# Optimization experiments

Hardware: AMD Instinct MI355X
Metric: run time of the kernel (lower is better)

The kernel has to match this reference:

```python
import jax, jax.numpy as jnp
import numpy as np

SEQ_LEN, BATCH, NUM_GROUPS, GROUP = 12, 512, 16, 32
H, E, MLP, BOTTLE, PRE = 128, 64, 1024, 1024, 512


def _pool_net(h, pos, num_groups, Wp, bp, W1, b1, W2, b2):
    # PoolHiddenNet: for each scene group, pairwise relative positions -> MLP -> max over neighbors
    B = h.shape[0]
    G = B // num_groups
    hg = h.reshape(num_groups, G, -1)          # (NG, G, H)
    pg = pos.reshape(num_groups, G, 2)         # (NG, G, 2)
    rel = pg[:, None, :, :] - pg[:, :, None, :]  # [g,i,j] = pos_j - pos_i
    emb = rel @ Wp.T + bp                      # (NG, G, G, E)
    hj = jnp.broadcast_to(hg[:, None, :, :], (num_groups, G, G, hg.shape[-1]))
    feats = jnp.concatenate([emb, hj], axis=-1)  # (NG, G, G, E+H)
    x = jax.nn.relu(feats @ W1.T + b1)         # (NG, G, G, 512)
    x = jax.nn.relu(x @ W2.T + b2)             # (NG, G, G, 1024)
    return x.max(axis=2).reshape(B, -1)        # max over neighbors j


def setup_inputs() -> dict:
    key = jax.random.key(0)
    ks = jax.random.split(key, 24)
    s = 0.05
    starts = np.arange(NUM_GROUPS, dtype=np.int64) * GROUP
    seq_start_end = jnp.asarray(np.stack([starts, starts + GROUP], axis=1))
    return {
        "last_pos": jax.random.normal(ks[0], (BATCH, 2), jnp.float32),
        "last_pos_rel": jax.random.normal(ks[1], (BATCH, 2), jnp.float32),
        "hh": jax.random.normal(ks[2], (1, BATCH, H), jnp.float32),
        "ch": jax.random.normal(ks[3], (1, BATCH, H), jnp.float32),
        "pred_traj_rel": jax.random.normal(ks[4], (SEQ_LEN, BATCH, 2), jnp.float32),
        "seq_start_end": seq_start_end,
        # LSTM (torch layout: gates ordered i,f,g,o)
        "W_ih": jax.random.normal(ks[5], (4 * H, E), jnp.float32) * s,
        "W_hh": jax.random.normal(ks[6], (4 * H, H), jnp.float32) * s,
        "b_ih": jax.random.normal(ks[7], (4 * H,), jnp.float32) * s,
        "b_hh": jax.random.normal(ks[8], (4 * H,), jnp.float32) * s,
        # spatial_embedding Linear(2, E)
        "Wse": jax.random.normal(ks[9], (E, 2), jnp.float32) * s,
        "bse": jax.random.normal(ks[10], (E,), jnp.float32) * s,
        # hidden2pos Linear(H, 2)
        "Wpos": jax.random.normal(ks[11], (2, H), jnp.float32) * s,
        "bpos": jax.random.normal(ks[12], (2,), jnp.float32) * s,
        # pool_net spatial_embedding Linear(2, E)
        "Wp": jax.random.normal(ks[13], (E, 2), jnp.float32) * s,
        "bp": jax.random.normal(ks[14], (E,), jnp.float32) * s,
        # pool_net mlp_pre_pool: [E+H, 512, BOTTLE], relu after each linear
        "W1": jax.random.normal(ks[15], (PRE, E + H), jnp.float32) * s,
        "b1": jax.random.normal(ks[16], (PRE,), jnp.float32) * s,
        "W2": jax.random.normal(ks[17], (BOTTLE, PRE), jnp.float32) * s,
        "b2": jax.random.normal(ks[18], (BOTTLE,), jnp.float32) * s,
        # decoder mlp: [H+BOTTLE, MLP, H], relu after each linear
        "Wm1": jax.random.normal(ks[19], (MLP, H + BOTTLE), jnp.float32) * s,
        "bm1": jax.random.normal(ks[20], (MLP,), jnp.float32) * s,
        "Wm2": jax.random.normal(ks[21], (H, MLP), jnp.float32) * s,
        "bm2": jax.random.normal(ks[22], (H,), jnp.float32) * s,
    }


def reference(last_pos, last_pos_rel, hh, ch, pred_traj_rel, seq_start_end,
              W_ih, W_hh, b_ih, b_hh, Wse, bse, Wpos, bpos,
              Wp, bp, W1, b1, W2, b2, Wm1, bm1, Wm2, bm2):
    num_groups = seq_start_end.shape[0]
    h0, c0 = hh[0], ch[0]
    dec_in0 = last_pos_rel @ Wse.T + bse

    def step(carry, gt_rel):
        last_pos_c, h, c, dec_in, loss = carry
        # single-layer LSTM cell (torch gate order i,f,g,o)
        gates = dec_in @ W_ih.T + b_ih + h @ W_hh.T + b_hh
        i, f, g, o = jnp.split(gates, 4, axis=-1)
        c = jax.nn.sigmoid(f) * c + jax.nn.sigmoid(i) * jnp.tanh(g)
        h = jax.nn.sigmoid(o) * jnp.tanh(c)
        rel_pos = h @ Wpos.T + bpos
        curr_pos = rel_pos + last_pos_c
        # pool every timestep + mlp back down to h_dim, replaces hidden state
        pool_h = _pool_net(h, curr_pos, num_groups, Wp, bp, W1, b1, W2, b2)
        dh = jnp.concatenate([h, pool_h], axis=1)
        dh = jax.nn.relu(dh @ Wm1.T + bm1)
        h = jax.nn.relu(dh @ Wm2.T + bm2)
        # training mode: teacher forcing + MSE loss
        loss = loss + jnp.mean((rel_pos - gt_rel) ** 2)
        dec_in = gt_rel @ Wse.T + bse
        return (curr_pos, h, c, dec_in, loss), rel_pos

    init = (last_pos, h0, c0, dec_in0, jnp.float32(0.0))
    (_, _, _, _, loss), pred_traj = jax.lax.scan(step, init, pred_traj_rel)
    return pred_traj, loss
```

## Files before the change

kernel.cpp:

```cpp
#include <hip/hip_runtime.h>
#include <math.h>

#define BATCH 512
#define NG 16
#define GSZ 32
#define H 128
#define E 64
#define PRE 512
#define BOT 1024
#define MLPD 1024
#define SEQ 12
#define AK 1152

typedef __attribute__((ext_vector_type(8))) short bf16x8;
typedef __attribute__((ext_vector_type(4))) float f32x4;

union bf8pack { ushort s[8]; uint4 v; };

__device__ __forceinline__ unsigned short f2bf(float f) {
    unsigned u = __float_as_uint(f);
    u += 0x7FFF + ((u >> 16) & 1);
    return (unsigned short)(u >> 16);
}

#define GLB(p) ((const __attribute__((address_space(1))) unsigned int*)(p))
#define LDS(p) ((__attribute__((address_space(3))) unsigned int*)(p))

#define N0 (BOT * PRE)
#define N1 (MLPD * AK)
#define N2 (H * MLPD)
#define N3 (PRE * H)
#define N4 (PRE)
#define N5 (BATCH * H)
#define N5b (BATCH * H)
#define N6 (BATCH * 2)
#define N7 (512 * 128)
#define N8 (512)
#define PREP_TOT (N0 + N1 + N2 + N3 + N4 + N5 + N5b + N6 + N7 + N8 + 1)

__global__ void prep_kernel(
    const float* __restrict__ W2, const float* __restrict__ Wm1,
    const float* __restrict__ Wm2, const float* __restrict__ W1,
    const float* __restrict__ Wp, const float* __restrict__ bp, const float* __restrict__ b1,
    const float* __restrict__ ch, const float* __restrict__ hh, const float* __restrict__ last_pos,
    const float* __restrict__ Wih, const float* __restrict__ Whh,
    const float* __restrict__ bih, const float* __restrict__ bhh,
    const float* __restrict__ Wse, const float* __restrict__ bse,
    unsigned short* __restrict__ W2pk, unsigned short* __restrict__ Wm1pk,
    unsigned short* __restrict__ Wm2pk, unsigned short* __restrict__ W1pk,
    float* __restrict__ Wcx, float* __restrict__ Wcy, float* __restrict__ biash,
    float* __restrict__ cbuf, float* __restrict__ hbuf, float* __restrict__ pos,
    unsigned short* __restrict__ Whpk,
    float* __restrict__ Wx0, float* __restrict__ Wx1, float* __restrict__ bx,
    float* __restrict__ loss)
{
    long idx = (long)blockIdx.x * 256 + threadIdx.x;
    if (idx < N0) {
        int e = (int)(idx & 7);
        long u = idx >> 3;
        int lane = (int)(u & 63);
        int rest = (int)(u >> 6);
        int ksg = rest & 15, cg = rest >> 4;
        int col = cg * 16 + (lane & 15);
        int kk = ksg * 32 + (lane >> 4) * 8 + e;
        W2pk[idx] = f2bf(W2[(size_t)col * PRE + kk]);
        return;
    }
    idx -= N0;
    if (idx < N1) {
        int e = (int)(idx & 7);
        long u = idx >> 3;
        int lane = (int)(u & 63);
        long rest = u >> 6;
        int ksg = (int)(rest % 36);
        int cg = (int)(rest / 36);
        int col = cg * 16 + (lane & 15);
        int k = ksg * 32 + (lane >> 4) * 8 + e;
        Wm1pk[idx] = f2bf(Wm1[(size_t)col * AK + k]);
        return;
    }
    idx -= N1;
    if (idx < N2) {
        int e = (int)(idx & 7);
        long u = idx >> 3;
        int lane = (int)(u & 63);
        int rest = (int)(u >> 6);
        int ksg = rest & 31, cg = rest >> 5;
        int col = cg * 16 + (lane & 15);
        int k = ksg * 32 + (lane >> 4) * 8 + e;
        Wm2pk[idx] = f2bf(Wm2[(size_t)col * MLPD + k]);
        return;
    }
    idx -= N2;
    if (idx < N3) {
        int e = (int)(idx & 7);
        int u = (int)(idx >> 3);
        int l16 = u & 15, quad = (u >> 4) & 3, nt = (u >> 6) & 3, ks = (u >> 8) & 3, w = u >> 10;
        int col = w * 64 + nt * 16 + l16;
        int k = ks * 32 + quad * 8 + e;
        W1pk[idx] = f2bf(W1[col * 192 + E + k]);
        return;
    }
    idx -= N3;
    if (idx < N4) {
        int p = (int)idx;
        float sx = 0.f, sy = 0.f, sb = 0.f;
#pragma unroll 8
        for (int e = 0; e < E; ++e) {
            float w = W1[p * 192 + e];
            sx += w * Wp[e * 2 + 0];
            sy += w * Wp[e * 2 + 1];
            sb += w * bp[e];
        }
        Wcx[p] = sx; Wcy[p] = sy; biash[p] = b1[p] + sb;
        return;
    }
    idx -= N4;
    if (idx < N5) { cbuf[idx] = ch[idx]; return; }
    idx -= N5;
    if (idx < N5b) { hbuf[idx] = hh[idx]; return; }
    idx -= N5b;
    if (idx < N6) { pos[idx] = last_pos[idx]; return; }
    idx -= N6;
    if (idx < N7) {
        int e = (int)(idx & 7);
        int u = (int)(idx >> 3);
        int l16 = u & 15, quad = (u >> 4) & 3, ks = (u >> 6) & 3, w = (u >> 8) & 7, g = u >> 11;
        int col = g * 128 + w * 16 + l16;
        int k = ks * 32 + quad * 8 + e;
        Whpk[idx] = f2bf(Whh[col * H + k]);
        return;
    }
    idx -= N7;
    if (idx < N8) {
        int u = (int)idx;
        float sx = 0.f, sy = 0.f, sb = 0.f;
#pragma unroll 8
        for (int e = 0; e < E; ++e) {
            float w = Wih[u * E + e];
            sx += w * Wse[e * 2 + 0];
            sy += w * Wse[e * 2 + 1];
            sb += w * bse[e];
        }
        Wx0[u] = sx; Wx1[u] = sy; bx[u] = sb + bih[u] + bhh[u];
        return;
    }
    idx -= N8;
    if (idx == 0) *loss = 0.0f;
}

#define LROWS 16
__global__ __launch_bounds__(512) void lstm_hpart(
    int t,
    const float* __restrict__ relin, const float* __restrict__ gt,
    const unsigned short* __restrict__ Whpk,
    const float* __restrict__ Wx0, const float* __restrict__ Wx1, const float* __restrict__ bx,
    const float* __restrict__ Wpos, const float* __restrict__ bpos,
    const unsigned short* __restrict__ W1pk, const float* __restrict__ biash,
    const float* __restrict__ hbuf, float* __restrict__ cbuf,
    unsigned short* __restrict__ Abf, float* __restrict__ Hpartf,
    float* __restrict__ pos, float* __restrict__ traj, float* __restrict__ loss)
{
    constexpr int LDHB = 136;
    constexpr int LDHF = 129;
    __shared__ __align__(16) unsigned short As[LROWS * LDHB];
    __shared__ __align__(16) unsigned short hnb[LROWS * LDHB];
    __shared__ float hnf[LROWS * LDHF];
    __shared__ float lred[8];
    const int r0 = blockIdx.x * LROWS;
    const int tid = threadIdx.x;
    const int lane = tid & 63, w = tid >> 6;
    const int quad = lane >> 4, l16 = lane & 15;

    for (int idx = tid; idx < LROWS * H; idx += 512) {
        int row = idx >> 7, k = idx & 127;
        As[row * LDHB + k] = f2bf(hbuf[(size_t)(r0 + row) * H + k]);
    }
    __syncthreads();

    f32x4 acc[4];
#pragma unroll
    for (int g4 = 0; g4 < 4; ++g4) acc[g4] = (f32x4)0.f;
#pragma unroll
    for (int ks = 0; ks < 4; ++ks) {
        bf16x8 af = *(const bf16x8*)&As[l16 * LDHB + ks * 32 + quad * 8];
#pragma unroll
        for (int gate = 0; gate < 4; ++gate) {
            bf16x8 bf = *(const bf16x8*)&Whpk[((size_t)((gate * 8 + w) * 4 + ks) * 64 + lane) * 8];
            acc[gate] = __builtin_amdgcn_mfma_f32_16x16x32_bf16(af, bf, acc[gate], 0, 0, 0);
        }
    }

    {
        int u = w * 16 + l16;
        float wx0[4], wx1[4], bxv[4];
#pragma unroll
        for (int gate = 0; gate < 4; ++gate) {
            int col = gate * 128 + u;
            wx0[gate] = Wx0[col]; wx1[gate] = Wx1[col]; bxv[gate] = bx[col];
        }
#pragma unroll
        for (int r = 0; r < 4; ++r) {
            int row = quad * 4 + r;
            int b = r0 + row;
            float rx = relin[b * 2 + 0], ry = relin[b * 2 + 1];
            float i_ = acc[0][r] + rx * wx0[0] + ry * wx1[0] + bxv[0];
            float f_ = acc[1][r] + rx * wx0[1] + ry * wx1[1] + bxv[1];
            float g_ = acc[2][r] + rx * wx0[2] + ry * wx1[2] + bxv[2];
            float o_ = acc[3][r] + rx * wx0[3] + ry * wx1[3] + bxv[3];
            float ig = 1.0f / (1.0f + expf(-i_));
            float fg = 1.0f / (1.0f + expf(-f_));
            float gg = tanhf(g_);
            float og = 1.0f / (1.0f + expf(-o_));
            float c = fg * cbuf[(size_t)b * H + u] + ig * gg;
            cbuf[(size_t)b * H + u] = c;
            float h = og * tanhf(c);
            hnb[row * LDHB + u] = f2bf(h);
            hnf[row * LDHF + u] = h;
            Abf[(size_t)b * AK + u] = f2bf(h);
        }
    }
    __syncthreads();

    if (t < SEQ - 1) {
        f32x4 acc2[4];
#pragma unroll
        for (int nt = 0; nt < 4; ++nt) acc2[nt] = (f32x4)0.f;
#pragma unroll
        for (int ks = 0; ks < 4; ++ks) {
            bf16x8 af = *(const bf16x8*)&hnb[l16 * LDHB + ks * 32 + quad * 8];
#pragma unroll
            for (int nt = 0; nt < 4; ++nt) {
                bf16x8 bfr = *(const bf16x8*)&W1pk[((size_t)((w * 4 + ks) * 4 + nt) * 64 + lane) * 8];
                acc2[nt] = __builtin_amdgcn_mfma_f32_16x16x32_bf16(af, bfr, acc2[nt], 0, 0, 0);
            }
        }
#pragma unroll
        for (int nt = 0; nt < 4; ++nt) {
            int col = w * 64 + nt * 16 + l16;
            float bv = biash[col];
#pragma unroll
            for (int r = 0; r < 4; ++r) {
                int row = quad * 4 + r;
                Hpartf[(size_t)(r0 + row) * PRE + col] = acc2[nt][r] + bv;
            }
        }
    }

    {
        int row = tid >> 5, o = (tid >> 4) & 1, seg = tid & 15;
        const float* wr = Wpos + o * H + seg * 8;
        const float* hr = &hnf[row * LDHF + seg * 8];
        float acc3 = 0.f;
#pragma unroll
        for (int k = 0; k < 8; ++k) acc3 += wr[k] * hr[k];
        acc3 += __shfl_xor(acc3, 1);
        acc3 += __shfl_xor(acc3, 2);
        acc3 += __shfl_xor(acc3, 4);
        acc3 += __shfl_xor(acc3, 8);
        acc3 += bpos[o];
        int b = r0 + row;
        float d = acc3 - gt[b * 2 + o];
        if (seg == 0) {
            float lp = pos[b * 2 + o];
            pos[b * 2 + o] = acc3 + lp;
            traj[b * 2 + o] = acc3;
        }
        float part = (seg == 0) ? d * d : 0.f;
        part += __shfl_xor(part, 16);
        part += __shfl_xor(part, 32);
        if (lane == 0) lred[w] = part;
        __syncthreads();
        if (tid == 0) {
            float s = 0.f;
#pragma unroll
            for (int i = 0; i < 8; ++i) s += lred[i];
            atomicAdd(loss, s * (1.0f / 1024.0f));
        }
    }
}

template <int BM, int BN, int KW, int NW, int MODE>
__global__ __launch_bounds__(256) void gemm_splitk_pk(
    const unsigned short* __restrict__ A, int lda,
    const unsigned short* __restrict__ Bpk, int K,
    const float* __restrict__ bias,
    float* __restrict__ Cf, unsigned short* __restrict__ Cb, int ldc)
{
    constexpr int MT = BM / 16;
    constexpr int NT = BN / (16 * NW);
    constexpr int ABUF = KW * BM * 64;
    __shared__ __align__(16) unsigned short As[2 * ABUF];
    __shared__ float red[KW * BM * BN];
    int tid = threadIdx.x;
    int lane = tid & 63, w = tid >> 6;
    int kslice = w / NW, nslice = w % NW;
    int gtid = tid & (NW * 64 - 1);
    int quad = lane >> 4, l16 = lane & 15;
    int m0 = blockIdx.y * BM, n0 = blockIdx.x * BN;
    const int KC = K / KW;
    const int NK = KC / 64;
    const int KSGT = K >> 5;
    const int cgbase = (n0 + nslice * (BN / NW)) >> 4;

    auto STAGE = [&](int ki, int bo) {
        int kb = kslice * KC + ki * 64;
#pragma unroll
        for (int u = 0; u < BM / (8 * NW); ++u) {
            int c = u * NW * 64 + gtid;
            __builtin_amdgcn_global_load_lds(
                GLB(A + (size_t)(m0 + (c >> 3)) * lda + kb + (c & 7) * 8),
                LDS(&As[bo + kslice * BM * 64 + c * 8]), 16, 0, 0);
        }
    };

    f32x4 acc[MT][NT];
#pragma unroll
    for (int mt = 0; mt < MT; ++mt)
#pragma unroll
        for (int nt = 0; nt < NT; ++nt) acc[mt][nt] = (f32x4)0.f;

    STAGE(0, 0);
    for (int ki = 0; ki < NK; ++ki) {
        int bo = (ki & 1) * ABUF;
        int kgbase = (kslice * KC + ki * 64) >> 5;
        __syncthreads();
#pragma unroll
        for (int ks = 0; ks < 2; ++ks) {
            bf16x8 af[MT], bfr[NT];
#pragma unroll
            for (int mt = 0; mt < MT; ++mt)
                af[mt] = *(const bf16x8*)&As[bo + kslice * BM * 64 + (mt * 16 + l16) * 64 + ks * 32 + quad * 8];
#pragma unroll
            for (int nt = 0; nt < NT; ++nt)
                bfr[nt] = *(const bf16x8*)&Bpk[((size_t)((cgbase + nt) * KSGT + kgbase + ks) * 64 + lane) * 8];
#pragma unroll
            for (int mt = 0; mt < MT; ++mt)
#pragma unroll
                for (int nt = 0; nt < NT; ++nt)
                    acc[mt][nt] = __builtin_amdgcn_mfma_f32_16x16x32_bf16(af[mt], bfr[nt], acc[mt][nt], 0, 0, 0);
        }
        if (ki + 1 < NK) STAGE(ki + 1, ((ki + 1) & 1) * ABUF);
    }

#pragma unroll
    for (int mt = 0; mt < MT; ++mt)
#pragma unroll
    for (int nt = 0; nt < NT; ++nt) {
#pragma unroll
        for (int r = 0; r < 4; ++r) {
            int row = mt * 16 + quad * 4 + r;
            int col = nslice * (BN / NW) + nt * 16 + l16;
            red[kslice * BM * BN + row * BN + col] = acc[mt][nt][r];
        }
    }
    __syncthreads();

#pragma unroll
    for (int o = 0; o < BM * BN / 256; ++o) {
        int e = o * 256 + tid;
        int row = e / BN, col = e % BN;
        float s = 0.f;
#pragma unroll
        for (int k = 0; k < KW; ++k) s += red[k * BM * BN + e];
        float v = fmaxf(s + bias[n0 + col], 0.f);
        if (MODE == 1) Cb[(size_t)(m0 + row) * ldc + n0 + col] = f2bf(v);
        else           Cf[(size_t)(m0 + row) * ldc + n0 + col] = v;
    }
}

__global__ __launch_bounds__(512) void pool_fused(
    const float* __restrict__ Hpartf, const float* __restrict__ pos,
    const float* __restrict__ Wcx, const float* __restrict__ Wcy,
    const unsigned short* __restrict__ W2pk,
    const float* __restrict__ b2, unsigned short* __restrict__ Abf)
{
    constexpr int LDA = 72;
    constexpr int ASZ = 128 * LDA;
    __shared__ __align__(16) unsigned short As[2 * ASZ];
    const int tid = threadIdx.x;
    const int lane = tid & 63, w = tid >> 6;
    const int quad = lane >> 4, l16 = lane & 15;
    const int n_tile = blockIdx.x, m_tile = blockIdx.y;
    const int g = m_tile >> 3, iq = m_tile & 7;
    const int n0 = n_tile * 512;

    const int brow = tid >> 2;
    const int k8 = (tid & 3) * 16;
    const int bi = iq * 4 + (brow >> 5), bj = brow & 31;
    const float rx = pos[(g * GSZ + bj) * 2 + 0] - pos[(g * GSZ + bi) * 2 + 0];
    const float ry = pos[(g * GSZ + bj) * 2 + 1] - pos[(g * GSZ + bi) * 2 + 1];
    const float* hrow = &Hpartf[(size_t)(g * GSZ + bj) * PRE];

    auto BUILD = [&](int k0i, unsigned short* dst) {
        const int k0 = k0i * 64;
        const float4* hp = (const float4*)(hrow + k0 + k8);
        const float4* wx = (const float4*)(Wcx + k0 + k8);
        const float4* wy = (const float4*)(Wcy + k0 + k8);
        bf8pack o[2];
#pragma unroll
        for (int q = 0; q < 2; ++q) {
            float4 ha = hp[q * 2], hb = hp[q * 2 + 1];
            float4 xa = wx[q * 2], xb = wx[q * 2 + 1];
            float4 ya = wy[q * 2], yb = wy[q * 2 + 1];
            o[q].s[0] = f2bf(fmaxf(ha.x + rx * xa.x + ry * ya.x, 0.f));
            o[q].s[1] = f2bf(fmaxf(ha.y + rx * xa.y + ry * ya.y, 0.f));
            o[q].s[2] = f2bf(fmaxf(ha.z + rx * xa.z + ry * ya.z, 0.f));
            o[q].s[3] = f2bf(fmaxf(ha.w + rx * xa.w + ry * ya.w, 0.f));
            o[q].s[4] = f2bf(fmaxf(hb.x + rx * xb.x + ry * yb.x, 0.f));
            o[q].s[5] = f2bf(fmaxf(hb.y + rx * xb.y + ry * yb.y, 0.f));
            o[q].s[6] = f2bf(fmaxf(hb.z + rx * xb.z + ry * yb.z, 0.f));
            o[q].s[7] = f2bf(fmaxf(hb.w + rx * xb.w + ry * yb.w, 0.f));
        }
        *(uint4*)&dst[brow * LDA + k8] = o[0].v;
        *(uint4*)&dst[brow * LDA + k8 + 8] = o[1].v;
    };

    f32x4 acc[8][4];
#pragma unroll
    for (int mt = 0; mt < 8; ++mt)
#pragma unroll
        for (int nt = 0; nt < 4; ++nt) acc[mt][nt] = (f32x4)0.f;

    BUILD(0, As);
    for (int k0i = 0; k0i < 8; ++k0i) {
        unsigned short* cur = As + (k0i & 1) * ASZ;
        __syncthreads();
#pragma unroll
        for (int ks = 0; ks < 2; ++ks) {
            bf16x8 bfr[4];
#pragma unroll
            for (int nt = 0; nt < 4; ++nt) {
                int cg = n_tile * 32 + w * 4 + nt;
                int ksg = k0i * 2 + ks;
                bfr[nt] = *(const bf16x8*)&W2pk[((size_t)(cg * 16 + ksg) * 64 + lane) * 8];
            }
#pragma unroll
            for (int mt = 0; mt < 8; ++mt) {
                bf16x8 af = *(const bf16x8*)&cur[(mt * 16 + l16) * LDA + ks * 32 + quad * 8];
#pragma unroll
                for (int nt = 0; nt < 4; ++nt)
                    acc[mt][nt] = __builtin_amdgcn_mfma_f32_16x16x32_bf16(af, bfr[nt], acc[mt][nt], 0, 0, 0);
            }
        }
        if (k0i < 7) BUILD(k0i + 1, As + ((k0i + 1) & 1) * ASZ);
    }

#pragma unroll
    for (int il = 0; il < 4; ++il)
#pragma unroll
    for (int nt = 0; nt < 4; ++nt) {
        float u = -1e30f;
#pragma unroll
        for (int p = 0; p < 2; ++p)
#pragma unroll
            for (int r = 0; r < 4; ++r) u = fmaxf(u, acc[il * 2 + p][nt][r]);
        u = fmaxf(u, __shfl_xor(u, 16));
        u = fmaxf(u, __shfl_xor(u, 32));
        if (lane < 16) {
            int col = n0 + w * 64 + nt * 16 + l16;
            int gu = m_tile * 4 + il;
            Abf[(size_t)gu * AK + H + col] = f2bf(fmaxf(u + b2[col], 0.f));
        }
    }
}

extern "C" void kernel_launch(void* const* d_in, const int* in_sizes, int n_in,
                              void* d_out, int out_size, void* d_ws, size_t ws_size,
                              hipStream_t stream)
{
    const float* last_pos     = (const float*)d_in[0];
    const float* last_pos_rel = (const float*)d_in[1];
    const float* hh           = (const float*)d_in[2];
    const float* ch           = (const float*)d_in[3];
    const float* ptr_rel      = (const float*)d_in[4];
    const float* Wih  = (const float*)d_in[6];
    const float* Whh  = (const float*)d_in[7];
    const float* bih  = (const float*)d_in[8];
    const float* bhh  = (const float*)d_in[9];
    const float* Wse  = (const float*)d_in[10];
    const float* bse  = (const float*)d_in[11];
    const float* Wpos = (const float*)d_in[12];
    const float* bpos = (const float*)d_in[13];
    const float* Wp   = (const float*)d_in[14];
    const float* bp   = (const float*)d_in[15];
    const float* W1   = (const float*)d_in[16];
    const float* b1   = (const float*)d_in[17];
    const float* W2   = (const float*)d_in[18];
    const float* b2   = (const float*)d_in[19];
    const float* Wm1  = (const float*)d_in[20];
    const float* bm1  = (const float*)d_in[21];
    const float* Wm2  = (const float*)d_in[22];
    const float* bm2  = (const float*)d_in[23];

    float* ws     = (float*)d_ws;
    float* hbuf   = ws;
    float* cbuf   = hbuf + BATCH * H;
    float* pos    = cbuf + BATCH * H;
    float* Hpartf = pos + 1024;
    float* Wcx    = Hpartf + BATCH * PRE;
    float* Wcy    = Wcx + PRE;
    float* biash  = Wcy + PRE;
    float* bx     = biash + PRE;
    float* Wx0    = bx + 512;
    float* Wx1    = Wx0 + 512;
    unsigned short* ub    = (unsigned short*)(Wx1 + 512);
    unsigned short* Abf   = ub;
    unsigned short* dhbf  = Abf + (size_t)BATCH * AK;
    unsigned short* W2pk  = dhbf + (size_t)BATCH * MLPD;
    unsigned short* Wm1pk = W2pk + (size_t)BOT * PRE;
    unsigned short* Wm2pk = Wm1pk + (size_t)MLPD * AK;
    unsigned short* W1pk  = Wm2pk + (size_t)H * MLPD;
    unsigned short* Whpk  = W1pk + (size_t)PRE * H;

    float* out  = (float*)d_out;
    float* loss = out + SEQ * BATCH * 2;

    prep_kernel<<<(PREP_TOT + 255) / 256, 256, 0, stream>>>(
        W2, Wm1, Wm2, W1, Wp, bp, b1, ch, hh, last_pos, Wih, Whh, bih, bhh, Wse, bse,
        W2pk, Wm1pk, Wm2pk, W1pk, Wcx, Wcy, biash, cbuf, hbuf, pos, Whpk, Wx0, Wx1, bx, loss);

    for (int t = 0; t < SEQ; t++) {
        const float* relin = (t == 0) ? last_pos_rel : (ptr_rel + (t - 1) * BATCH * 2);
        const float* gt = ptr_rel + t * BATCH * 2;
        lstm_hpart<<<BATCH / LROWS, 512, 0, stream>>>(t, relin, gt, Whpk, Wx0, Wx1, bx,
                                                      Wpos, bpos, W1pk, biash, hbuf, cbuf,
                                                      Abf, Hpartf, pos,
                                                      out + t * BATCH * 2, loss);
        if (t == SEQ - 1) break;
        pool_fused<<<dim3(2, 128), 512, 0, stream>>>(Hpartf, pos, Wcx, Wcy, W2pk, b2, Abf);
        gemm_splitk_pk<64, 32, 2, 2, 1><<<dim3(MLPD / 32, BATCH / 64), 256, 0, stream>>>(
            Abf, AK, Wm1pk, AK, bm1, nullptr, dhbf, MLPD);
        gemm_splitk_pk<16, 32, 4, 1, 2><<<dim3(H / 32, BATCH / 16), 256, 0, stream>>>(
            dhbf, MLPD, Wm2pk, MLPD, bm2, hbuf, nullptr, H);
    }
}
```

Before: 668.9 us.

## Store hidden state as pre-packed bf16 MFMA fragments; vectorize prep; raise MFMA priority

The Wm2 GEMM epilogue now writes the new hidden state directly as bf16 in the MFMA A-fragment layout. The LSTM kernel therefore loads its A operands straight from global memory, with no fp32 load, bf16 convert, LDS staging pass or barrier. The prep kernel packs eight elements per thread with vectorized float4 loads and uint4 stores, and it packs the initial hidden state the same way. s_setprio is raised around the MFMA loop in the pool kernel. The trade-off is scattered 2-byte stores in the GEMM epilogue, and the hidden state is held only in bf16.

```diff
diff --git a/kernel.cpp b/kernel.cpp
--- a/kernel.cpp
+++ b/kernel.cpp
@@ -23,20 +23,28 @@
     return (unsigned short)(u >> 16);
 }
 
+__device__ __forceinline__ uint4 pack8(const float* s) {
+    float4 a = *(const float4*)s, b = *(const float4*)(s + 4);
+    bf8pack o;
+    o.s[0] = f2bf(a.x); o.s[1] = f2bf(a.y); o.s[2] = f2bf(a.z); o.s[3] = f2bf(a.w);
+    o.s[4] = f2bf(b.x); o.s[5] = f2bf(b.y); o.s[6] = f2bf(b.z); o.s[7] = f2bf(b.w);
+    return o.v;
+}
+
 #define GLB(p) ((const __attribute__((address_space(1))) unsigned int*)(p))
 #define LDS(p) ((__attribute__((address_space(3))) unsigned int*)(p))
 
-#define N0 (BOT * PRE)
-#define N1 (MLPD * AK)
-#define N2 (H * MLPD)
-#define N3 (PRE * H)
-#define N4 (PRE)
-#define N5 (BATCH * H)
-#define N5b (BATCH * H)
-#define N6 (BATCH * 2)
-#define N7 (512 * 128)
-#define N8 (512)
-#define PREP_TOT (N0 + N1 + N2 + N3 + N4 + N5 + N5b + N6 + N7 + N8 + 1)
+#define U0 ((BOT * PRE) / 8)
+#define U1 ((MLPD * AK) / 8)
+#define U2 ((H * MLPD) / 8)
+#define U3 ((PRE * H) / 8)
+#define U4 (PRE)
+#define U5 ((BATCH * H) / 4)
+#define U5b ((BATCH * H) / 8)
+#define U6 (BATCH * 2)
+#define U7 ((512 * 128) / 8)
+#define U8 (512)
+#define PREP_TOT (U0 + U1 + U2 + U3 + U4 + U5 + U5b + U6 + U7 + U8 + 1)
 
 __global__ void prep_kernel(
     const float* __restrict__ W2, const float* __restrict__ Wm1,
@@ -49,60 +57,52 @@
     unsigned short* __restrict__ W2pk, unsigned short* __restrict__ Wm1pk,
     unsigned short* __restrict__ Wm2pk, unsigned short* __restrict__ W1pk,
     float* __restrict__ Wcx, float* __restrict__ Wcy, float* __restrict__ biash,
-    float* __restrict__ cbuf, float* __restrict__ hbuf, float* __restrict__ pos,
+    float* __restrict__ cbuf, unsigned short* __restrict__ Ahpk, float* __restrict__ pos,
     unsigned short* __restrict__ Whpk,
     float* __restrict__ Wx0, float* __restrict__ Wx1, float* __restrict__ bx,
     float* __restrict__ loss)
 {
     long idx = (long)blockIdx.x * 256 + threadIdx.x;
-    if (idx < N0) {
-        int e = (int)(idx & 7);
-        long u = idx >> 3;
-        int lane = (int)(u & 63);
-        int rest = (int)(u >> 6);
+    if (idx < U0) {
+        int u = (int)idx;
+        int lane = u & 63, rest = u >> 6;
         int ksg = rest & 15, cg = rest >> 4;
         int col = cg * 16 + (lane & 15);
-        int kk = ksg * 32 + (lane >> 4) * 8 + e;
-        W2pk[idx] = f2bf(W2[(size_t)col * PRE + kk]);
-        return;
-    }
-    idx -= N0;
-    if (idx < N1) {
-        int e = (int)(idx & 7);
-        long u = idx >> 3;
-        int lane = (int)(u & 63);
-        long rest = u >> 6;
-        int ksg = (int)(rest % 36);
-        int cg = (int)(rest / 36);
+        int kk = ksg * 32 + (lane >> 4) * 8;
+        *(uint4*)&W2pk[(size_t)u * 8] = pack8(&W2[(size_t)col * PRE + kk]);
+        return;
+    }
+    idx -= U0;
+    if (idx < U1) {
+        int u = (int)idx;
+        int lane = u & 63, rest = u >> 6;
+        int ksg = rest % 36, cg = rest / 36;
         int col = cg * 16 + (lane & 15);
-        int k = ksg * 32 + (lane >> 4) * 8 + e;
-        Wm1pk[idx] = f2bf(Wm1[(size_t)col * AK + k]);
-        return;
-    }
-    idx -= N1;
-    if (idx < N2) {
-        int e = (int)(idx & 7);
-        long u = idx >> 3;
-        int lane = (int)(u & 63);
-        int rest = (int)(u >> 6);
+        int k = ksg * 32 + (lane >> 4) * 8;
+        *(uint4*)&Wm1pk[(size_t)u * 8] = pack8(&Wm1[(size_t)col * AK + k]);
+        return;
+    }
+    idx -= U1;
+    if (idx < U2) {
+        int u = (int)idx;
+        int lane = u & 63, rest = u >> 6;
         int ksg = rest & 31, cg = rest >> 5;
         int col = cg * 16 + (lane & 15);
-        int k = ksg * 32 + (lane >> 4) * 8 + e;
-        Wm2pk[idx] = f2bf(Wm2[(size_t)col * MLPD + k]);
-        return;
-    }
-    idx -= N2;
-    if (idx < N3) {
-        int e = (int)(idx & 7);
-        int u = (int)(idx >> 3);
+        int k = ksg * 32 + (lane >> 4) * 8;
+        *(uint4*)&Wm2pk[(size_t)u * 8] = pack8(&Wm2[(size_t)col * MLPD + k]);
+        return;
+    }
+    idx -= U2;
+    if (idx < U3) {
+        int u = (int)idx;
         int l16 = u & 15, quad = (u >> 4) & 3, nt = (u >> 6) & 3, ks = (u >> 8) & 3, w = u >> 10;
         int col = w * 64 + nt * 16 + l16;
-        int k = ks * 32 + quad * 8 + e;
-        W1pk[idx] = f2bf(W1[col * 192 + E + k]);
-        return;
-    }
-    idx -= N3;
-    if (idx < N4) {
+        int k = ks * 32 + quad * 8;
+        *(uint4*)&W1pk[(size_t)u * 8] = pack8(&W1[col * 192 + E + k]);
+        return;
+    }
+    idx -= U3;
+    if (idx < U4) {
         int p = (int)idx;
         float sx = 0.f, sy = 0.f, sb = 0.f;
 #pragma unroll 8
@@ -115,24 +115,31 @@
         Wcx[p] = sx; Wcy[p] = sy; biash[p] = b1[p] + sb;
         return;
     }
-    idx -= N4;
-    if (idx < N5) { cbuf[idx] = ch[idx]; return; }
-    idx -= N5;
-    if (idx < N5b) { hbuf[idx] = hh[idx]; return; }
-    idx -= N5b;
-    if (idx < N6) { pos[idx] = last_pos[idx]; return; }
-    idx -= N6;
-    if (idx < N7) {
-        int e = (int)(idx & 7);
-        int u = (int)(idx >> 3);
+    idx -= U4;
+    if (idx < U5) { ((float4*)cbuf)[idx] = ((const float4*)ch)[idx]; return; }
+    idx -= U5;
+    if (idx < U5b) {
+        int u = (int)idx;
+        int lane = u & 63, rest = u >> 6;
+        int ks = rest & 3, rowtile = rest >> 2;
+        int row = rowtile * 16 + (lane & 15);
+        int k = ks * 32 + (lane >> 4) * 8;
+        *(uint4*)&Ahpk[(size_t)u * 8] = pack8(&hh[(size_t)row * H + k]);
+        return;
+    }
+    idx -= U5b;
+    if (idx < U6) { pos[idx] = last_pos[idx]; return; }
+    idx -= U6;
+    if (idx < U7) {
+        int u = (int)idx;
         int l16 = u & 15, quad = (u >> 4) & 3, ks = (u >> 6) & 3, w = (u >> 8) & 7, g = u >> 11;
         int col = g * 128 + w * 16 + l16;
-        int k = ks * 32 + quad * 8 + e;
-        Whpk[idx] = f2bf(Whh[col * H + k]);
-        return;
-    }
-    idx -= N7;
-    if (idx < N8) {
+        int k = ks * 32 + quad * 8;
+        *(uint4*)&Whpk[(size_t)u * 8] = pack8(&Whh[(size_t)col * H + k]);
+        return;
+    }
+    idx -= U7;
+    if (idx < U8) {
         int u = (int)idx;
         float sx = 0.f, sy = 0.f, sb = 0.f;
 #pragma unroll 8
@@ -145,7 +152,7 @@
         Wx0[u] = sx; Wx1[u] = sy; bx[u] = sb + bih[u] + bhh[u];
         return;
     }
-    idx -= N8;
+    idx -= U8;
     if (idx == 0) *loss = 0.0f;
 }
 
@@ -157,33 +164,27 @@
     const float* __restrict__ Wx0, const float* __restrict__ Wx1, const float* __restrict__ bx,
     const float* __restrict__ Wpos, const float* __restrict__ bpos,
     const unsigned short* __restrict__ W1pk, const float* __restrict__ biash,
-    const float* __restrict__ hbuf, float* __restrict__ cbuf,
+    const unsigned short* __restrict__ Ahpk, float* __restrict__ cbuf,
     unsigned short* __restrict__ Abf, float* __restrict__ Hpartf,
     float* __restrict__ pos, float* __restrict__ traj, float* __restrict__ loss)
 {
     constexpr int LDHB = 136;
     constexpr int LDHF = 129;
-    __shared__ __align__(16) unsigned short As[LROWS * LDHB];
     __shared__ __align__(16) unsigned short hnb[LROWS * LDHB];
     __shared__ float hnf[LROWS * LDHF];
     __shared__ float lred[8];
-    const int r0 = blockIdx.x * LROWS;
+    const int blk = blockIdx.x;
+    const int r0 = blk * LROWS;
     const int tid = threadIdx.x;
     const int lane = tid & 63, w = tid >> 6;
     const int quad = lane >> 4, l16 = lane & 15;
 
-    for (int idx = tid; idx < LROWS * H; idx += 512) {
-        int row = idx >> 7, k = idx & 127;
-        As[row * LDHB + k] = f2bf(hbuf[(size_t)(r0 + row) * H + k]);
-    }
-    __syncthreads();
-
     f32x4 acc[4];
 #pragma unroll
     for (int g4 = 0; g4 < 4; ++g4) acc[g4] = (f32x4)0.f;
 #pragma unroll
     for (int ks = 0; ks < 4; ++ks) {
-        bf16x8 af = *(const bf16x8*)&As[l16 * LDHB + ks * 32 + quad * 8];
+        bf16x8 af = *(const bf16x8*)&Ahpk[((size_t)(blk * 4 + ks) * 64 + lane) * 8];
 #pragma unroll
         for (int gate = 0; gate < 4; ++gate) {
             bf16x8 bf = *(const bf16x8*)&Whpk[((size_t)((gate * 8 + w) * 4 + ks) * 64 + lane) * 8];
@@ -364,8 +365,17 @@
 #pragma unroll
         for (int k = 0; k < KW; ++k) s += red[k * BM * BN + e];
         float v = fmaxf(s + bias[n0 + col], 0.f);
-        if (MODE == 1) Cb[(size_t)(m0 + row) * ldc + n0 + col] = f2bf(v);
-        else           Cf[(size_t)(m0 + row) * ldc + n0 + col] = v;
+        if (MODE == 1) {
+            Cb[(size_t)(m0 + row) * ldc + n0 + col] = f2bf(v);
+        } else if (MODE == 2) {
+            Cf[(size_t)(m0 + row) * ldc + n0 + col] = v;
+        } else {
+            int gr = m0 + row, gc = n0 + col;
+            int rowtile = gr >> 4, l16p = gr & 15;
+            int ksv = gc >> 5, quadp = (gc >> 3) & 3, ep = gc & 7;
+            int lanep = quadp * 16 + l16p;
+            Cb[((size_t)(rowtile * 4 + ksv) * 64 + lanep) * 8 + ep] = f2bf(v);
+        }
     }
 }
 
@@ -426,6 +436,7 @@
     for (int k0i = 0; k0i < 8; ++k0i) {
         unsigned short* cur = As + (k0i & 1) * ASZ;
         __syncthreads();
+        __builtin_amdgcn_s_setprio(1);
 #pragma unroll
         for (int ks = 0; ks < 2; ++ks) {
             bf16x8 bfr[4];
@@ -443,6 +454,7 @@
                     acc[mt][nt] = __builtin_amdgcn_mfma_f32_16x16x32_bf16(af, bfr[nt], acc[mt][nt], 0, 0, 0);
             }
         }
+        __builtin_amdgcn_s_setprio(0);
         if (k0i < 7) BUILD(k0i + 1, As + ((k0i + 1) & 1) * ASZ);
     }
 
@@ -494,8 +506,8 @@
     const float* bm2  = (const float*)d_in[23];
 
     float* ws     = (float*)d_ws;
-    float* hbuf   = ws;
-    float* cbuf   = hbuf + BATCH * H;
+    unsigned short* Ahpk = (unsigned short*)ws;
+    float* cbuf   = ws + BATCH * H;
     float* pos    = cbuf + BATCH * H;
     float* Hpartf = pos + 1024;
     float* Wcx    = Hpartf + BATCH * PRE;
@@ -518,20 +530,20 @@
 
     prep_kernel<<<(PREP_TOT + 255) / 256, 256, 0, stream>>>(
         W2, Wm1, Wm2, W1, Wp, bp, b1, ch, hh, last_pos, Wih, Whh, bih, bhh, Wse, bse,
-        W2pk, Wm1pk, Wm2pk, W1pk, Wcx, Wcy, biash, cbuf, hbuf, pos, Whpk, Wx0, Wx1, bx, loss);
+        W2pk, Wm1pk, Wm2pk, W1pk, Wcx, Wcy, biash, cbuf, Ahpk, pos, Whpk, Wx0, Wx1, bx, loss);
 
     for (int t = 0; t < SEQ; t++) {
         const float* relin = (t == 0) ? last_pos_rel : (ptr_rel + (t - 1) * BATCH * 2);
         const float* gt = ptr_rel + t * BATCH * 2;
         lstm_hpart<<<BATCH / LROWS, 512, 0, stream>>>(t, relin, gt, Whpk, Wx0, Wx1, bx,
-                                                      Wpos, bpos, W1pk, biash, hbuf, cbuf,
+                                                      Wpos, bpos, W1pk, biash, Ahpk, cbuf,
                                                       Abf, Hpartf, pos,
                                                       out + t * BATCH * 2, loss);
         if (t == SEQ - 1) break;
         pool_fused<<<dim3(2, 128), 512, 0, stream>>>(Hpartf, pos, Wcx, Wcy, W2pk, b2, Abf);
         gemm_splitk_pk<64, 32, 2, 2, 1><<<dim3(MLPD / 32, BATCH / 64), 256, 0, stream>>>(
             Abf, AK, Wm1pk, AK, bm1, nullptr, dhbf, MLPD);
-        gemm_splitk_pk<16, 32, 4, 1, 2><<<dim3(H / 32, BATCH / 16), 256, 0, stream>>>(
-            dhbf, MLPD, Wm2pk, MLPD, bm2, hbuf, nullptr, H);
-    }
-}
+        gemm_splitk_pk<16, 32, 4, 1, 3><<<dim3(H / 32, BATCH / 16), 256, 0, stream>>>(
+            dhbf, MLPD, Wm2pk, MLPD, bm2, nullptr, Ahpk, H);
+    }
+}
```

Result: no change. 665.1 us (-0.6%).
